# Kernel optimization log

Measured on AMD Instinct MI355X. Metric: run time of the kernel, lower is better.

## Reference

```python
import jax, jax.numpy as jnp
import numpy as np
import math

N_HEAD = 16

def setup_inputs() -> dict:
    key = jax.random.key(0)
    k1, k2, k3 = jax.random.split(key, 3)
    B, S, D = 4, 2048, 1024
    x = jax.random.normal(k1, (B, S, D), dtype=jnp.float32)
    w_attn = jax.random.normal(k2, (3 * D, D), dtype=jnp.float32) * 0.02
    b_attn = jnp.zeros((3 * D,), dtype=jnp.float32)
    w_proj = jax.random.normal(k3, (D, D), dtype=jnp.float32) * 0.02
    b_proj = jnp.zeros((D,), dtype=jnp.float32)
    return {"x": x, "w_attn": w_attn, "b_attn": b_attn, "w_proj": w_proj, "b_proj": b_proj}


def reference(x, w_attn, b_attn, w_proj, b_proj):
    B, S, D = x.shape
    H = N_HEAD
    hd = D // H
    # c_attn: nn.Linear -> x @ W^T + b, then split into q,k,v
    qkv = x @ w_attn.T + b_attn                      # [B,S,3D]
    q, k, v = jnp.split(qkv, 3, axis=-1)
    # split heads -> [B,H,S,hd]
    q = q.reshape(B, S, H, hd).transpose(0, 2, 1, 3)
    k = k.reshape(B, S, H, hd).transpose(0, 2, 1, 3)
    v = v.reshape(B, S, H, hd).transpose(0, 2, 1, 3)
    # scaled causal attention (scale=True divides by sqrt(head_dim))
    scores = jnp.einsum('bhqd,bhkd->bhqk', q, k) / math.sqrt(hd)
    mask = jnp.tril(jnp.ones((S, S), dtype=bool))
    scores = jnp.where(mask[None, None], scores, jnp.float32(-1e10))
    w = jax.nn.softmax(scores, axis=-1)
    a = jnp.einsum('bhqk,bhkd->bhqd', w, v)          # [B,H,S,hd]
    # merge heads
    a = a.transpose(0, 2, 1, 3).reshape(B, S, D)
    # c_proj: Conv1D -> x @ W + b with W [nx, nf]
    out = a @ w_proj + b_proj
    # present = stack(key [B,H,S,hd], value [B,H,S,hd])
    present = jnp.stack((k, v))
    return out, present
```

## Files before the change

### kernel.cpp

```cpp
#include <hip/hip_runtime.h>
#include <hip/hip_bf16.h>
#include <stdint.h>

typedef unsigned short u16t;
typedef short s8v __attribute__((ext_vector_type(8)));
typedef float f32x4 __attribute__((ext_vector_type(4)));

#define BB 4
#define SS 2048
#define DD 1024
#define HH 16
#define HD 64
#define MROWS (BB*SS)
#define OUT_ELEMS (MROWS*DD)
#define KV_ELEMS (MROWS*DD)

__device__ __forceinline__ u16t f2bf(float f) {
  union { float f; unsigned int u; } v; v.f = f;
  unsigned int u = v.u;
  unsigned int r = (u + 0x7FFFu + ((u >> 16) & 1u)) >> 16;
  return (u16t)r;
}

__device__ __forceinline__ void async_copy16(u16t* lds_dst, const u16t* g_src) {
  __builtin_amdgcn_global_load_lds(
      (const __attribute__((address_space(1))) unsigned int*)(g_src),
      (__attribute__((address_space(3))) unsigned int*)(lds_dst),
      16, 0, 0);
}

__global__ void convert_f32_bf16(const float* __restrict__ in, u16t* __restrict__ out) {
  int i = (blockIdx.x * blockDim.x + threadIdx.x) * 4;
  float4 f = *(const float4*)(in + i);
  ushort4 o;
  o.x = f2bf(f.x); o.y = f2bf(f.y); o.z = f2bf(f.z); o.w = f2bf(f.w);
  *(ushort4*)(out + i) = o;
}

__global__ void transpose_to_bf16(const float* __restrict__ W, u16t* __restrict__ WT) {
  __shared__ float tile[64][65];
  int bx = blockIdx.x & 15;
  int by = blockIdx.x >> 4;
  int t = threadIdx.x;
  int c = t & 63, r0 = t >> 6;
  for (int i = 0; i < 16; i++) {
    int r = r0 * 16 + i;
    tile[r][c] = W[(size_t)(by*64 + r)*1024 + bx*64 + c];
  }
  __syncthreads();
  for (int i = 0; i < 16; i++) {
    int r = r0 * 16 + i;
    WT[(size_t)(bx*64 + r)*1024 + by*64 + c] = f2bf(tile[c][r]);
  }
}

template<int MODE>
__global__ __launch_bounds__(256)
void gemm_bt(const u16t* __restrict__ A, const u16t* __restrict__ Bm,
             const float* __restrict__ bias, float* __restrict__ outF,
             u16t* __restrict__ qb, u16t* __restrict__ kb, u16t* __restrict__ vb,
             float* __restrict__ presK, float* __restrict__ presV,
             int M, int N, int K) {
  __shared__ u16t As[128*32];
  __shared__ u16t Bs[128*32];
  int tiles_n = N >> 7;
  int cpx = gridDim.x >> 3;
  int wg = (blockIdx.x & 7) * cpx + (blockIdx.x >> 3);
  int bm = wg / tiles_n, bn = wg % tiles_n;
  int t = threadIdx.x;
  int w = t >> 6, l = t & 63;
  int wm = (w >> 1) * 64, wn = (w & 1) * 64;
  int lr = l & 15, lg = l >> 4;
  int r4 = l >> 2, c8 = (l & 3) * 8;
  const u16t* Ab = A  + (size_t)(bm * 128) * K;
  const u16t* Bb = Bm + (size_t)(bn * 128) * K;

  f32x4 acc[4][4] = {};

  for (int k0 = 0; k0 < K; k0 += 32) {
    __syncthreads();
    async_copy16(As + w*512,        Ab + (size_t)(w*16 + r4)*K      + k0 + c8);
    async_copy16(As + 2048 + w*512, Ab + (size_t)(64 + w*16 + r4)*K + k0 + c8);
    async_copy16(Bs + w*512,        Bb + (size_t)(w*16 + r4)*K      + k0 + c8);
    async_copy16(Bs + 2048 + w*512, Bb + (size_t)(64 + w*16 + r4)*K + k0 + c8);
    __syncthreads();
    s8v a[4], b[4];
#pragma unroll
    for (int mf = 0; mf < 4; mf++) a[mf] = *(s8v*)&As[(wm + mf*16 + lr)*32 + lg*8];
#pragma unroll
    for (int nf = 0; nf < 4; nf++) b[nf] = *(s8v*)&Bs[(wn + nf*16 + lr)*32 + lg*8];
#pragma unroll
    for (int mf = 0; mf < 4; mf++)
#pragma unroll
      for (int nf = 0; nf < 4; nf++)
        acc[mf][nf] = __builtin_amdgcn_mfma_f32_16x16x32_bf16(a[mf], b[nf], acc[mf][nf], 0, 0, 0);
  }

#pragma unroll
  for (int mf = 0; mf < 4; mf++)
#pragma unroll
    for (int nf = 0; nf < 4; nf++)
#pragma unroll
      for (int j = 0; j < 4; j++) {
        int m = bm*128 + wm + mf*16 + lg*4 + j;
        int n = bn*128 + wn + nf*16 + lr;
        float val = acc[mf][nf][j] + bias[n];
        if (MODE == 1) {
          outF[(size_t)m * N + n] = val;
        } else {
          int part = n >> 10, nn = n & 1023;
          int h = nn >> 6, d = nn & 63;
          int bi = m >> 11, s = m & 2047;
          size_t idx = ((size_t)(bi*HH + h)*SS + s)*HD + d;
          if (part == 0) {
            qb[idx] = f2bf(val * 0.125f);
          } else if (part == 1) {
            kb[idx] = f2bf(val); presK[idx] = val;
          } else {
            vb[((size_t)(bi*HH + h)*HD + d)*SS + s] = f2bf(val);
            presV[idx] = val;
          }
        }
      }
}

__global__ __launch_bounds__(256, 5)
void attn_kernel(const u16t* __restrict__ qb, const u16t* __restrict__ kb,
                 const u16t* __restrict__ vtb, u16t* __restrict__ ab) {
  __shared__ u16t Ks[2][64*64];
  __shared__ u16t Vs[2][64*64];

  int bid = blockIdx.x;
  int logical = (bid & 7) * 256 + (bid >> 3);
  int bh = logical >> 5;
  int qt = 31 - (logical & 31);
  int q0 = qt * 64;
  int t = threadIdx.x, w = t >> 6, l = t & 63;
  int lr = l & 15, lg = l >> 4;
  const u16t* Qg = qb  + (size_t)bh * SS * HD;
  const u16t* Kg = kb  + (size_t)bh * SS * HD;
  const u16t* Vg = vtb + (size_t)bh * HD * SS;

  int Rrow = t >> 3;
  int csrc = (((t & 7) ^ ((t >> 3) & 7))) * 8;

  s8v qa0 = *(const s8v*)&Qg[(size_t)(q0 + w*16 + lr)*HD + lg*8];
  s8v qa1 = *(const s8v*)&Qg[(size_t)(q0 + w*16 + lr)*HD + 32 + lg*8];

  f32x4 o[4] = {};
  float m_ = -1e30f, l_ = 0.f;

  auto swz = [](int R, int c) { return R*64 + ((c ^ (R & 7)) << 3); };

  int nt = qt + 1;
#pragma unroll
  for (int r = 0; r < 2; r++) {
    async_copy16(&Ks[0][(size_t)(r*256 + w*64) * 8], Kg + (size_t)(r*32 + Rrow)*HD + csrc);
    async_copy16(&Vs[0][(size_t)(r*256 + w*64) * 8], Vg + (size_t)(r*32 + Rrow)*SS + csrc);
  }
  __syncthreads();

  int src0 = (l & 15) | ((l & 16) << 1);
  int src1 = src0 + 16;
  bool hi = (l & 32) != 0;

  int cur = 0;
  for (int tt = 0; tt < nt; tt++) {
    int kv0 = tt * 64;
    if (tt + 1 < nt) {
      int kn = kv0 + 64;
#pragma unroll
      for (int r = 0; r < 2; r++) {
        async_copy16(&Ks[cur^1][(size_t)(r*256 + w*64) * 8], Kg + (size_t)(kn + r*32 + Rrow)*HD + csrc);
        async_copy16(&Vs[cur^1][(size_t)(r*256 + w*64) * 8], Vg + (size_t)(r*32 + Rrow)*SS + kn + csrc);
      }
    }

    const u16t* Kt = Ks[cur];
    const u16t* Vt = Vs[cur];

    f32x4 s[4];
#pragma unroll
    for (int nf = 0; nf < 4; nf++) {
      int R = nf*16 + lr;
      s8v bk0 = *(const s8v*)&Kt[swz(R, lg)];
      s8v bk1 = *(const s8v*)&Kt[swz(R, 4 + lg)];
      f32x4 a = {};
      a = __builtin_amdgcn_mfma_f32_16x16x32_bf16(bk0, qa0, a, 0, 0, 0);
      a = __builtin_amdgcn_mfma_f32_16x16x32_bf16(bk1, qa1, a, 0, 0, 0);
      s[nf] = a;
    }
    if (tt == qt) {
      int qrow = w*16 + lr;
#pragma unroll
      for (int nf = 0; nf < 4; nf++)
#pragma unroll
        for (int j = 0; j < 4; j++) {
          int kv = nf*16 + lg*4 + j;
          if (kv > qrow) s[nf][j] = -1e30f;
        }
    }

    float pmax = s[0][0];
#pragma unroll
    for (int nf = 0; nf < 4; nf++)
#pragma unroll
      for (int j = 0; j < 4; j++) pmax = fmaxf(pmax, s[nf][j]);
    pmax = fmaxf(pmax, __shfl_xor(pmax, 16));
    pmax = fmaxf(pmax, __shfl_xor(pmax, 32));

    if (!__all(pmax <= m_ + 8.0f)) {
      float mnew = fmaxf(m_, pmax);
      float r_ = __expf(m_ - mnew);
      m_ = mnew;
      l_ *= r_;
      float r0f = __shfl(r_, 4*lg + 0);
      float r1f = __shfl(r_, 4*lg + 1);
      float r2f = __shfl(r_, 4*lg + 2);
      float r3f = __shfl(r_, 4*lg + 3);
#pragma unroll
      for (int nf = 0; nf < 4; nf++) {
        o[nf][0] *= r0f; o[nf][1] *= r1f; o[nf][2] *= r2f; o[nf][3] *= r3f;
      }
    }

    float psum = 0.f;
#pragma unroll
    for (int nf = 0; nf < 4; nf++)
#pragma unroll
      for (int j = 0; j < 4; j++) {
        float p = __expf(s[nf][j] - m_);
        s[nf][j] = p;
        psum += p;
      }
    psum += __shfl_xor(psum, 16);
    psum += __shfl_xor(psum, 32);
    l_ += psum;

    uint32_t s01[4], s23[4];
#pragma unroll
    for (int nf = 0; nf < 4; nf++) {
      asm("v_cvt_pk_bf16_f32 %0, %1, %2" : "=v"(s01[nf]) : "v"(s[nf][0]), "v"(s[nf][1]));
      asm("v_cvt_pk_bf16_f32 %0, %1, %2" : "=v"(s23[nf]) : "v"(s[nf][2]), "v"(s[nf][3]));
    }
    union PU { s8v v; uint32_t w[4]; } pa0, pa1;
    {
      uint32_t t00 = __shfl(s01[0], src0), t01 = __shfl(s01[1], src0);
      uint32_t t10 = __shfl(s23[0], src0), t11 = __shfl(s23[1], src0);
      uint32_t t20 = __shfl(s01[0], src1), t21 = __shfl(s01[1], src1);
      uint32_t t30 = __shfl(s23[0], src1), t31 = __shfl(s23[1], src1);
      pa0.w[0] = hi ? t01 : t00; pa0.w[1] = hi ? t11 : t10;
      pa0.w[2] = hi ? t21 : t20; pa0.w[3] = hi ? t31 : t30;
      uint32_t u00 = __shfl(s01[2], src0), u01 = __shfl(s01[3], src0);
      uint32_t u10 = __shfl(s23[2], src0), u11 = __shfl(s23[3], src0);
      uint32_t u20 = __shfl(s01[2], src1), u21 = __shfl(s01[3], src1);
      uint32_t u30 = __shfl(s23[2], src1), u31 = __shfl(s23[3], src1);
      pa1.w[0] = hi ? u01 : u00; pa1.w[1] = hi ? u11 : u10;
      pa1.w[2] = hi ? u21 : u20; pa1.w[3] = hi ? u31 : u30;
    }

#pragma unroll
    for (int nf = 0; nf < 4; nf++) {
      int R = nf*16 + lr;
      s8v vv0 = *(const s8v*)&Vt[swz(R, lg)];
      s8v vv1 = *(const s8v*)&Vt[swz(R, 4 + lg)];
      o[nf] = __builtin_amdgcn_mfma_f32_16x16x32_bf16(pa0.v, vv0, o[nf], 0, 0, 0);
      o[nf] = __builtin_amdgcn_mfma_f32_16x16x32_bf16(pa1.v, vv1, o[nf], 0, 0, 0);
    }

    __syncthreads();
    cur ^= 1;
  }

  float li0 = 1.f / __shfl(l_, 4*lg + 0);
  float li1 = 1.f / __shfl(l_, 4*lg + 1);
  float li2 = 1.f / __shfl(l_, 4*lg + 2);
  float li3 = 1.f / __shfl(l_, 4*lg + 3);
  int bi = bh >> 4, h = bh & 15;
#pragma unroll
  for (int nf = 0; nf < 4; nf++) {
    int row = q0 + w*16 + lg*4;
    int col = h*HD + nf*16 + lr;
    ab[((size_t)bi*SS + row + 0)*DD + col] = f2bf(o[nf][0] * li0);
    ab[((size_t)bi*SS + row + 1)*DD + col] = f2bf(o[nf][1] * li1);
    ab[((size_t)bi*SS + row + 2)*DD + col] = f2bf(o[nf][2] * li2);
    ab[((size_t)bi*SS + row + 3)*DD + col] = f2bf(o[nf][3] * li3);
  }
}

extern "C" void kernel_launch(void* const* d_in, const int* in_sizes, int n_in,
                              void* d_out, int out_size, void* d_ws, size_t ws_size,
                              hipStream_t stream) {
  const float* x      = (const float*)d_in[0];
  const float* w_attn = (const float*)d_in[1];
  const float* b_attn = (const float*)d_in[2];
  const float* w_proj = (const float*)d_in[3];
  const float* b_proj = (const float*)d_in[4];
  float* out   = (float*)d_out;
  float* presK = out + (size_t)OUT_ELEMS;
  float* presV = presK + (size_t)KV_ELEMS;

  u16t* ws    = (u16t*)d_ws;
  u16t* x_bf  = ws;
  u16t* wa_bf = x_bf  + (size_t)OUT_ELEMS;
  u16t* wpT   = wa_bf + 3145728;
  u16t* q_bf  = wpT   + 1048576;
  u16t* k_bf  = q_bf  + (size_t)KV_ELEMS;
  u16t* vt_bf = k_bf  + (size_t)KV_ELEMS;
  u16t* a_bf  = x_bf;

  convert_f32_bf16<<<8192, 256, 0, stream>>>(x, x_bf);
  convert_f32_bf16<<<3072, 256, 0, stream>>>(w_attn, wa_bf);
  transpose_to_bf16<<<256, 256, 0, stream>>>(w_proj, wpT);

  gemm_bt<0><<<64*24, 256, 0, stream>>>(x_bf, wa_bf, b_attn, nullptr,
                                        q_bf, k_bf, vt_bf, presK, presV,
                                        MROWS, 3*DD, DD);
  attn_kernel<<<64*32, 256, 0, stream>>>(q_bf, k_bf, vt_bf, a_bf);
  gemm_bt<1><<<64*8, 256, 0, stream>>>(a_bf, wpT, b_proj, out,
                                       nullptr, nullptr, nullptr, nullptr, nullptr,
                                       MROWS, DD, DD);
}
```

Baseline: 352.7 us.

## Deepen GEMM K-tile to 64 with XOR-swizzled LDS and narrower proj tiles

The GEMM now stages 64-wide K slices instead of 32, which halves the number of barrier pairs per tile. The LDS layout is XOR-swizzled so the 16-byte MFMA fragment reads avoid bank conflicts. The output projection uses 128x64 tiles, doubling its grid to 1024 blocks to fill more CUs, and launch bounds now request 4 waves per SIMD. In exchange, LDS use per block rises and the proj GEMM reloads A tiles more often.

Result: no change. 355.1 us (+0.7%).

```diff
diff --git a/kernel.cpp b/kernel.cpp
--- a/kernel.cpp
+++ b/kernel.cpp
@@ -54,56 +54,69 @@
   }
 }
 
-template<int MODE>
-__global__ __launch_bounds__(256)
+template<int MODE, int NF>
+__global__ __launch_bounds__(256, 4)
 void gemm_bt(const u16t* __restrict__ A, const u16t* __restrict__ Bm,
              const float* __restrict__ bias, float* __restrict__ outF,
              u16t* __restrict__ qb, u16t* __restrict__ kb, u16t* __restrict__ vb,
              float* __restrict__ presK, float* __restrict__ presV,
              int M, int N, int K) {
-  __shared__ u16t As[128*32];
-  __shared__ u16t Bs[128*32];
-  int tiles_n = N >> 7;
+  __shared__ u16t As[128*64];
+  __shared__ u16t Bs[NF*32*64];
+  const int TN = NF*32;
+  int tiles_n = N / TN;
   int cpx = gridDim.x >> 3;
   int wg = (blockIdx.x & 7) * cpx + (blockIdx.x >> 3);
   int bm = wg / tiles_n, bn = wg % tiles_n;
   int t = threadIdx.x;
   int w = t >> 6, l = t & 63;
-  int wm = (w >> 1) * 64, wn = (w & 1) * 64;
+  int wm = (w >> 1) * 64, wn = (w & 1) * (NF*16);
   int lr = l & 15, lg = l >> 4;
-  int r4 = l >> 2, c8 = (l & 3) * 8;
+  int Rrow = t >> 3;
+  int csrc = ((t & 7) ^ ((t >> 3) & 7)) * 8;
   const u16t* Ab = A  + (size_t)(bm * 128) * K;
-  const u16t* Bb = Bm + (size_t)(bn * 128) * K;
-
-  f32x4 acc[4][4] = {};
-
-  for (int k0 = 0; k0 < K; k0 += 32) {
+  const u16t* Bb = Bm + (size_t)(bn * TN) * K;
+
+  f32x4 acc[4][NF] = {};
+
+  for (int k0 = 0; k0 < K; k0 += 64) {
     __syncthreads();
-    async_copy16(As + w*512,        Ab + (size_t)(w*16 + r4)*K      + k0 + c8);
-    async_copy16(As + 2048 + w*512, Ab + (size_t)(64 + w*16 + r4)*K + k0 + c8);
-    async_copy16(Bs + w*512,        Bb + (size_t)(w*16 + r4)*K      + k0 + c8);
-    async_copy16(Bs + 2048 + w*512, Bb + (size_t)(64 + w*16 + r4)*K + k0 + c8);
+#pragma unroll
+    for (int r = 0; r < 4; r++)
+      async_copy16(&As[(size_t)(r*256 + t)*8], Ab + (size_t)(r*32 + Rrow)*K + k0 + csrc);
+#pragma unroll
+    for (int r = 0; r < NF; r++)
+      async_copy16(&Bs[(size_t)(r*256 + t)*8], Bb + (size_t)(r*32 + Rrow)*K + k0 + csrc);
     __syncthreads();
-    s8v a[4], b[4];
-#pragma unroll
-    for (int mf = 0; mf < 4; mf++) a[mf] = *(s8v*)&As[(wm + mf*16 + lr)*32 + lg*8];
-#pragma unroll
-    for (int nf = 0; nf < 4; nf++) b[nf] = *(s8v*)&Bs[(wn + nf*16 + lr)*32 + lg*8];
-#pragma unroll
-    for (int mf = 0; mf < 4; mf++)
-#pragma unroll
-      for (int nf = 0; nf < 4; nf++)
-        acc[mf][nf] = __builtin_amdgcn_mfma_f32_16x16x32_bf16(a[mf], b[nf], acc[mf][nf], 0, 0, 0);
+#pragma unroll
+    for (int kk = 0; kk < 2; kk++) {
+      s8v a[4], b[NF];
+#pragma unroll
+      for (int mf = 0; mf < 4; mf++) {
+        int R = wm + mf*16 + lr;
+        a[mf] = *(s8v*)&As[R*64 + (((kk*4 + lg) ^ (R & 7)) << 3)];
+      }
+#pragma unroll
+      for (int nf = 0; nf < NF; nf++) {
+        int R = wn + nf*16 + lr;
+        b[nf] = *(s8v*)&Bs[R*64 + (((kk*4 + lg) ^ (R & 7)) << 3)];
+      }
+#pragma unroll
+      for (int mf = 0; mf < 4; mf++)
+#pragma unroll
+        for (int nf = 0; nf < NF; nf++)
+          acc[mf][nf] = __builtin_amdgcn_mfma_f32_16x16x32_bf16(a[mf], b[nf], acc[mf][nf], 0, 0, 0);
+    }
   }
 
 #pragma unroll
   for (int mf = 0; mf < 4; mf++)
 #pragma unroll
-    for (int nf = 0; nf < 4; nf++)
+    for (int nf = 0; nf < NF; nf++)
 #pragma unroll
       for (int j = 0; j < 4; j++) {
         int m = bm*128 + wm + mf*16 + lg*4 + j;
-        int n = bn*128 + wn + nf*16 + lr;
+        int n = bn*TN + wn + nf*16 + lr;
         float val = acc[mf][nf][j] + bias[n];
         if (MODE == 1) {
           outF[(size_t)m * N + n] = val;
@@ -313,11 +326,11 @@
   convert_f32_bf16<<<3072, 256, 0, stream>>>(w_attn, wa_bf);
   transpose_to_bf16<<<256, 256, 0, stream>>>(w_proj, wpT);
 
-  gemm_bt<0><<<64*24, 256, 0, stream>>>(x_bf, wa_bf, b_attn, nullptr,
-                                        q_bf, k_bf, vt_bf, presK, presV,
-                                        MROWS, 3*DD, DD);
+  gemm_bt<0,4><<<64*24, 256, 0, stream>>>(x_bf, wa_bf, b_attn, nullptr,
+                                          q_bf, k_bf, vt_bf, presK, presV,
+                                          MROWS, 3*DD, DD);
   attn_kernel<<<64*32, 256, 0, stream>>>(q_bf, k_bf, vt_bf, a_bf);
-  gemm_bt<1><<<64*8, 256, 0, stream>>>(a_bf, wpT, b_proj, out,
-                                       nullptr, nullptr, nullptr, nullptr, nullptr,
-                                       MROWS, DD, DD);
-}
+  gemm_bt<1,2><<<128*8, 256, 0, stream>>>(a_bf, wpT, b_proj, out,
+                                          nullptr, nullptr, nullptr, nullptr, nullptr,
+                                          MROWS, DD, DD);
+}
```
